# Kernel optimization log

Hardware: AMD Instinct MI355X
Metric: run time of the kernel (lower is better)

## Reference

```python
import jax, jax.numpy as jnp
import numpy as np
from functools import partial

# Norse ConstantCurrentLIFEncoderCell defaults
TAU_SYN_INV = 1.0 / 5e-3   # 200.0
TAU_MEM_INV = 1.0 / 1e-2   # 100.0
V_LEAK = 0.0
V_TH = 1.0
V_RESET = 0.0
DT = 0.001


def setup_inputs() -> dict:
    key = jax.random.key(0)
    c, h, w = 3, 640, 640
    inp = jax.random.uniform(key, (c, h, w), dtype=jnp.float32)
    return {"input": inp, "steps": 32}


def reference(input, steps):
    # LIF feed-forward step with constant input current, scanned over time.
    zeros = jnp.zeros_like(input)

    def step(carry, _):
        v, i = carry
        # membrane integrates synaptic current, synaptic current decays
        v_decayed = v + DT * TAU_MEM_INV * ((V_LEAK - v) + i)
        i_decayed = i + DT * TAU_SYN_INV * (-i)
        z = (v_decayed - V_TH > 0).astype(jnp.float32)  # heaviside spike
        v_new = (1.0 - z) * v_decayed + z * V_RESET      # reset on spike
        i_new = i_decayed + input                        # constant current inject
        return (v_new, i_new), z

    _, events = jax.lax.scan(step, (zeros, zeros), None, length=steps)
    # events: [steps, c, h, w] float32 spike trains
    return events
```

## Files before the change

### kernel.cpp

```cpp
#include <hip/hip_runtime.h>


__global__ __launch_bounds__(256) void CurrentEncode_57286273794981_kernel(
    const float4* __restrict__ in4, float* __restrict__ out,
    int n, int steps) {
  const int n4 = n >> 2;
  const int nblk_per_half = (n4 + 255) >> 8;
  const int half = blockIdx.x / nblk_per_half;
  const int gid = (blockIdx.x - half * nblk_per_half) * 256 + threadIdx.x;
  if (gid >= n4) return;

  const int split = (steps + 1) >> 1;
  const int t0 = half ? split : 0;
  const int t1 = half ? steps : split;

  const float4 xin = in4[gid];
  float x[4] = {xin.x, xin.y, xin.z, xin.w};
  float v[4] = {0.0f, 0.0f, 0.0f, 0.0f};
  float c[4] = {0.0f, 0.0f, 0.0f, 0.0f};

  float4* out4 = reinterpret_cast<float4*>(out);

  for (int t = 0; t < t0; ++t) {
#pragma unroll
    for (int j = 0; j < 4; ++j) {
      float tmp = __fadd_rn(__fsub_rn(0.0f, v[j]), c[j]);
      float vd  = __fadd_rn(v[j], __fmul_rn(0.1f, tmp));
      float id  = __fadd_rn(c[j], __fmul_rn(0.2f, __fsub_rn(0.0f, c[j])));
      bool spike = (__fsub_rn(vd, 1.0f) > 0.0f);
      v[j] = spike ? 0.0f : vd;
      c[j] = __fadd_rn(id, x[j]);
    }
  }

  for (int t = t0; t < t1; ++t) {
    float z[4];
#pragma unroll
    for (int j = 0; j < 4; ++j) {
      float tmp = __fadd_rn(__fsub_rn(0.0f, v[j]), c[j]);
      float vd  = __fadd_rn(v[j], __fmul_rn(0.1f, tmp));
      float id  = __fadd_rn(c[j], __fmul_rn(0.2f, __fsub_rn(0.0f, c[j])));
      bool spike = (__fsub_rn(vd, 1.0f) > 0.0f);
      z[j] = spike ? 1.0f : 0.0f;
      v[j] = spike ? 0.0f : vd;
      c[j] = __fadd_rn(id, x[j]);
    }
    out4[(size_t)t * n4 + gid] = make_float4(z[0], z[1], z[2], z[3]);
  }
}

extern "C" void kernel_launch(void* const* d_in, const int* in_sizes, int n_in,
                              void* d_out, int out_size, void* d_ws, size_t ws_size,
                              hipStream_t stream) {
  const float* in = (const float*)d_in[0];
  float* out = (float*)d_out;
  const int n = in_sizes[0];
  const int steps = out_size / n;
  const int n4 = n >> 2;
  const int block = 256;
  const int nblk_per_half = (n4 + block - 1) / block;
  const int grid = nblk_per_half * 2;
  CurrentEncode_57286273794981_kernel<<<grid, block, 0, stream>>>(
      (const float4*)in, out, n, steps);
}
```

Before: 28.75 us.

## Drop time-split halves and fully unroll the 32-step LIF loop

Result: slower. 35.35 us (+23.0%).

```diff
diff --git a/kernel.cpp b/kernel.cpp
--- a/kernel.cpp
+++ b/kernel.cpp
@@ -1,18 +1,11 @@
 #include <hip/hip_runtime.h>
 
 
-__global__ __launch_bounds__(256) void CurrentEncode_57286273794981_kernel(
-    const float4* __restrict__ in4, float* __restrict__ out,
-    int n, int steps) {
-  const int n4 = n >> 2;
-  const int nblk_per_half = (n4 + 255) >> 8;
-  const int half = blockIdx.x / nblk_per_half;
-  const int gid = (blockIdx.x - half * nblk_per_half) * 256 + threadIdx.x;
+template <int STEPS>
+__global__ __launch_bounds__(256) void lif_encode_kernel(
+    const float4* __restrict__ in4, float* __restrict__ out, int n4) {
+  const int gid = blockIdx.x * 256 + threadIdx.x;
   if (gid >= n4) return;
-
-  const int split = (steps + 1) >> 1;
-  const int t0 = half ? split : 0;
-  const int t1 = half ? steps : split;
 
   const float4 xin = in4[gid];
   float x[4] = {xin.x, xin.y, xin.z, xin.w};
@@ -21,19 +14,34 @@
 
   float4* out4 = reinterpret_cast<float4*>(out);
 
-  for (int t = 0; t < t0; ++t) {
+#pragma unroll
+  for (int t = 0; t < STEPS; ++t) {
+    float z[4];
 #pragma unroll
     for (int j = 0; j < 4; ++j) {
       float tmp = __fadd_rn(__fsub_rn(0.0f, v[j]), c[j]);
       float vd  = __fadd_rn(v[j], __fmul_rn(0.1f, tmp));
       float id  = __fadd_rn(c[j], __fmul_rn(0.2f, __fsub_rn(0.0f, c[j])));
       bool spike = (__fsub_rn(vd, 1.0f) > 0.0f);
+      z[j] = spike ? 1.0f : 0.0f;
       v[j] = spike ? 0.0f : vd;
       c[j] = __fadd_rn(id, x[j]);
     }
+    out4[(size_t)t * n4 + gid] = make_float4(z[0], z[1], z[2], z[3]);
   }
+}
 
-  for (int t = t0; t < t1; ++t) {
+__global__ __launch_bounds__(256) void lif_encode_kernel_rt(
+    const float4* __restrict__ in4, float* __restrict__ out, int n4,
+    int steps) {
+  const int gid = blockIdx.x * 256 + threadIdx.x;
+  if (gid >= n4) return;
+  const float4 xin = in4[gid];
+  float x[4] = {xin.x, xin.y, xin.z, xin.w};
+  float v[4] = {0.0f, 0.0f, 0.0f, 0.0f};
+  float c[4] = {0.0f, 0.0f, 0.0f, 0.0f};
+  float4* out4 = reinterpret_cast<float4*>(out);
+  for (int t = 0; t < steps; ++t) {
     float z[4];
 #pragma unroll
     for (int j = 0; j < 4; ++j) {
@@ -58,8 +66,12 @@
   const int steps = out_size / n;
   const int n4 = n >> 2;
   const int block = 256;
-  const int nblk_per_half = (n4 + block - 1) / block;
-  const int grid = nblk_per_half * 2;
-  CurrentEncode_57286273794981_kernel<<<grid, block, 0, stream>>>(
-      (const float4*)in, out, n, steps);
+  const int grid = (n4 + block - 1) / block;
+  if (steps == 32) {
+    lif_encode_kernel<32><<<grid, block, 0, stream>>>(
+        (const float4*)in, out, n4);
+  } else {
+    lif_encode_kernel_rt<<<grid, block, 0, stream>>>(
+        (const float4*)in, out, n4, steps);
+  }
 }
```
